# Kernel optimization log

Measured on AMD Instinct MI355X. Metric: run time of the kernel, lower is better.

Reference implementation:

```python
import jax, jax.numpy as jnp
import numpy as np

N_ENTS = 100000
N_EDGES = 200000
H = 256
NUM_RELS = 200  # embedding table has 2*NUM_RELS rows
TYPE_DIM = H // 4


def layer_norm(x, g, b, eps=1e-5):
    m = jnp.mean(x, axis=-1, keepdims=True)
    v = jnp.var(x, axis=-1, keepdims=True)
    return (x - m) * jax.lax.rsqrt(v + eps) * g + b


def setup_inputs() -> dict:
    key = jax.random.key(0)
    ks = jax.random.split(key, 20)
    s = 0.02  # xavier-ish scale for weights
    return {
        "node_emb": jax.random.normal(ks[0], (N_ENTS, H), jnp.float32),
        "h_prev": jax.random.normal(ks[1], (N_ENTS, H), jnp.float32),
        "type_emb": jax.random.normal(ks[2], (2 * NUM_RELS, TYPE_DIM), jnp.float32) * s,
        "W_edge": jax.random.normal(ks[3], (2 * H + TYPE_DIM, H), jnp.float32) * s,
        "b_edge": jnp.zeros((H,), jnp.float32),
        "ln_edge_g": jnp.ones((H,), jnp.float32),
        "ln_edge_b": jnp.zeros((H,), jnp.float32),
        "W_gate": jax.random.normal(ks[4], (2 * H, H), jnp.float32) * s,
        "b_gate": jnp.zeros((H,), jnp.float32),
        "ln_gate_g": jnp.ones((H,), jnp.float32),
        "ln_gate_b": jnp.zeros((H,), jnp.float32),
        "W_ih": jax.random.normal(ks[5], (3 * H, H), jnp.float32) * s,
        "W_hh": jax.random.normal(ks[6], (3 * H, H), jnp.float32) * s,
        "b_ih": jnp.zeros((3 * H,), jnp.float32),
        "b_hh": jnp.zeros((3 * H,), jnp.float32),
        "ln_gru_g": jnp.ones((H,), jnp.float32),
        "ln_gru_b": jnp.zeros((H,), jnp.float32),
        "src": jax.random.randint(ks[7], (N_EDGES,), 0, N_ENTS, jnp.int32),
        "dst": jax.random.randint(ks[8], (N_EDGES,), 0, N_ENTS, jnp.int32),
        "edge_types": jax.random.randint(ks[9], (N_EDGES,), 0, 2 * NUM_RELS, jnp.int32),
    }


def reference(node_emb, h_prev, type_emb, W_edge, b_edge, ln_edge_g, ln_edge_b,
              W_gate, b_gate, ln_gate_g, ln_gate_b,
              W_ih, W_hh, b_ih, b_hh, ln_gru_g, ln_gru_b,
              src, dst, edge_types):
    # --- EdgeFeatureExtractor: gather + edge MLP (dropout=eval identity) ---
    edge_in = jnp.concatenate(
        [node_emb[src], node_emb[dst], type_emb[edge_types]], axis=1)  # [E, 2H+H/4]
    edge_feat = jax.nn.relu(
        layer_norm(edge_in @ W_edge + b_edge, ln_edge_g, ln_edge_b))  # [E, H]

    # --- create_edge_enhanced_nodes: scatter-mean over dst ---
    agg = jax.ops.segment_sum(edge_feat, dst, num_segments=N_ENTS)  # [N, H]
    cnt = jax.ops.segment_sum(jnp.ones((edge_feat.shape[0],), edge_feat.dtype),
                              dst, num_segments=N_ENTS)
    edge_enh = agg / jnp.clip(cnt, 1.0)[:, None]

    # --- DualStreamProcessor fusion ---
    gate = jax.nn.sigmoid(layer_norm(
        jnp.concatenate([node_emb, edge_enh], axis=1) @ W_gate + b_gate,
        ln_gate_g, ln_gate_b))
    fused = gate * node_emb + (1.0 - gate) * edge_enh
    x = 0.2 * node_emb + 0.8 * fused

    # --- EnhancedGRUCell: torch GRUCell + LayerNorm + 0.3*h residual ---
    gi = x @ W_ih.T + b_ih      # [N, 3H]
    gh = h_prev @ W_hh.T + b_hh  # [N, 3H]
    gi_r, gi_z, gi_n = jnp.split(gi, 3, axis=1)
    gh_r, gh_z, gh_n = jnp.split(gh, 3, axis=1)
    r = jax.nn.sigmoid(gi_r + gh_r)
    z = jax.nn.sigmoid(gi_z + gh_z)
    n = jnp.tanh(gi_n + r * gh_n)
    h = (1.0 - z) * n + z * h_prev
    h = layer_norm(h, ln_gru_g, ln_gru_b) + 0.3 * h_prev
    return h
```

## Files before the change

### kernel.cpp

```cpp
#include <hip/hip_runtime.h>
#include <hip/hip_bf16.h>
#include <hip/hip_fp16.h>

#define H 256
#define TYPE_DIM 64
#define EIN (2*H + TYPE_DIM)
#define N_ENTS 100000
#define N_EDGES 200000
#define EPB 32
#define NPB 64
#define KE 576
#define LDE 584
#define LDF 260
#define LDA 520
#define LDH 264
#define LDF2 260

typedef __hip_bfloat16 bf16;
typedef short bf16x8 __attribute__((ext_vector_type(8)));
typedef float f32x4 __attribute__((ext_vector_type(4)));

__device__ __forceinline__ unsigned short f2b(float f) {
    union { float f; unsigned int u; } v; v.f = f;
    unsigned int u = v.u;
    return (unsigned short)((u + 0x7FFFu + ((u >> 16) & 1u)) >> 16);
}
__device__ __forceinline__ unsigned int pack2(float a, float b) {
    return (unsigned int)f2b(a) | ((unsigned int)f2b(b) << 16);
}
__device__ __forceinline__ float u2f(unsigned short u) {
    union { unsigned int i; float f; } t; t.i = ((unsigned int)u) << 16; return t.f;
}
__device__ __forceinline__ float sigm(float x) { return 1.0f / (1.0f + __expf(-x)); }

__device__ __forceinline__ void atomic_pk_f16(void* p, unsigned int v) {
    asm volatile("global_atomic_pk_add_f16 %0, %1, off" :: "v"(p), "v"(v) : "memory");
}

__device__ __forceinline__ bf16x8 cvt8(const float* p) {
    f32x4 a = *(const f32x4*)p;
    f32x4 b = *(const f32x4*)(p + 4);
    union { bf16 h[8]; bf16x8 v; } u;
    u.h[0] = __float2bfloat16(a[0]); u.h[1] = __float2bfloat16(a[1]);
    u.h[2] = __float2bfloat16(a[2]); u.h[3] = __float2bfloat16(a[3]);
    u.h[4] = __float2bfloat16(b[0]); u.h[5] = __float2bfloat16(b[1]);
    u.h[6] = __float2bfloat16(b[2]); u.h[7] = __float2bfloat16(b[3]);
    return u.v;
}

__global__ void transpose_we(const float* __restrict__ W,
                             unsigned short* __restrict__ WE) {
    int c = blockIdx.x;
    for (int j = threadIdx.x; j < KE; j += 256)
        WE[(size_t)c * KE + j] = f2b(W[(size_t)j * H + c]);
}

__global__ void transpose_wg(const float* __restrict__ W,
                             unsigned short* __restrict__ WG) {
    int c = blockIdx.x;
    for (int k = threadIdx.x; k < 2 * H; k += 256)
        WG[(size_t)c * (2 * H) + k] = f2b(W[(size_t)k * H + c]);
}

__global__ void cast_gru(const float* __restrict__ Wih, const float* __restrict__ Whh,
                         unsigned short* __restrict__ WTih,
                         unsigned short* __restrict__ WThh, int do_hh) {
    int j = blockIdx.x;
    int k = threadIdx.x;
    WTih[(size_t)j * H + k] = f2b(Wih[(size_t)j * H + k]);
    if (do_hh) WThh[(size_t)j * H + k] = f2b(Whh[(size_t)j * H + k]);
}

__global__ __launch_bounds__(256) void edge_mfma(
    const float* __restrict__ node_emb, const float* __restrict__ type_emb,
    const unsigned short* __restrict__ WE,
    const float* __restrict__ b_edge,
    const float* __restrict__ ln_g, const float* __restrict__ ln_b,
    const int* __restrict__ src, const int* __restrict__ dst,
    const int* __restrict__ et,
    unsigned char* __restrict__ aggb,
    unsigned int* __restrict__ cntw) {
    __shared__ __align__(16) unsigned short ein[EPB * LDE];
    __shared__ int sidx[EPB], didx[EPB], tidx[EPB];

    const int tid = threadIdx.x;
    const int e0 = blockIdx.x * EPB;
    const int lane = tid & 63;
    const int w = tid >> 6;
    const int l15 = lane & 15;
    const int l4 = lane >> 4;

    if (tid < EPB) {
        sidx[tid] = src[e0 + tid];
        didx[tid] = dst[e0 + tid];
        tidx[tid] = et[e0 + tid];
    }
    __syncthreads();

    {
        const int half = tid >> 7;
        const int tt = tid & 127;
        #pragma unroll 4
        for (int e = 0; e < EPB; e++) {
            const int n = half ? didx[e] : sidx[e];
            const float2 v = *(const float2*)(node_emb + (size_t)n * H + 2 * tt);
            *(unsigned int*)&ein[e * LDE + half * 256 + 2 * tt] = pack2(v.x, v.y);
        }
        #pragma unroll
        for (int i = tid; i < EPB * 32; i += 256) {
            const int e = i >> 5, j = i & 31;
            const float2 v = *(const float2*)(type_emb + (size_t)tidx[e] * TYPE_DIM + 2 * j);
            *(unsigned int*)&ein[e * LDE + 512 + 2 * j] = pack2(v.x, v.y);
        }
    }
    __syncthreads();

    f32x4 acc[2][4];
    #pragma unroll
    for (int mt = 0; mt < 2; mt++)
        #pragma unroll
        for (int nt = 0; nt < 4; nt++)
            acc[mt][nt] = (f32x4){0.f, 0.f, 0.f, 0.f};

    const int colbase = w * 64;
    const unsigned short* A0 = &ein[l15 * LDE + l4 * 8];
    const unsigned short* A1 = &ein[(16 + l15) * LDE + l4 * 8];
    const unsigned short* B0 = WE + (size_t)(colbase + l15) * KE + l4 * 8;
    const unsigned short* B1 = B0 + 16 * KE;
    const unsigned short* B2 = B0 + 32 * KE;
    const unsigned short* B3 = B0 + 48 * KE;

    for (int ks = 0; ks < KE / 32; ks++) {
        const int o = ks * 32;
        bf16x8 a0 = __builtin_bit_cast(bf16x8, *(const uint4*)(A0 + o));
        bf16x8 a1 = __builtin_bit_cast(bf16x8, *(const uint4*)(A1 + o));
        bf16x8 b0 = __builtin_bit_cast(bf16x8, *(const uint4*)(B0 + o));
        bf16x8 b1 = __builtin_bit_cast(bf16x8, *(const uint4*)(B1 + o));
        bf16x8 b2 = __builtin_bit_cast(bf16x8, *(const uint4*)(B2 + o));
        bf16x8 b3 = __builtin_bit_cast(bf16x8, *(const uint4*)(B3 + o));
        acc[0][0] = __builtin_amdgcn_mfma_f32_16x16x32_bf16(a0, b0, acc[0][0], 0, 0, 0);
        acc[0][1] = __builtin_amdgcn_mfma_f32_16x16x32_bf16(a0, b1, acc[0][1], 0, 0, 0);
        acc[0][2] = __builtin_amdgcn_mfma_f32_16x16x32_bf16(a0, b2, acc[0][2], 0, 0, 0);
        acc[0][3] = __builtin_amdgcn_mfma_f32_16x16x32_bf16(a0, b3, acc[0][3], 0, 0, 0);
        acc[1][0] = __builtin_amdgcn_mfma_f32_16x16x32_bf16(a1, b0, acc[1][0], 0, 0, 0);
        acc[1][1] = __builtin_amdgcn_mfma_f32_16x16x32_bf16(a1, b1, acc[1][1], 0, 0, 0);
        acc[1][2] = __builtin_amdgcn_mfma_f32_16x16x32_bf16(a1, b2, acc[1][2], 0, 0, 0);
        acc[1][3] = __builtin_amdgcn_mfma_f32_16x16x32_bf16(a1, b3, acc[1][3], 0, 0, 0);
    }

    __syncthreads();
    float* fout = (float*)&ein[0];

    float bias[4];
    #pragma unroll
    for (int nt = 0; nt < 4; nt++) bias[nt] = b_edge[colbase + nt * 16 + l15];
    #pragma unroll
    for (int mt = 0; mt < 2; mt++)
        #pragma unroll
        for (int nt = 0; nt < 4; nt++)
            #pragma unroll
            for (int r = 0; r < 4; r++) {
                int row = mt * 16 + l4 * 4 + r;
                fout[row * LDF + colbase + nt * 16 + l15] = acc[mt][nt][r] + bias[nt];
            }
    __syncthreads();

    const float4 gv = *(const float4*)(ln_g + 4 * lane);
    const float4 bv = *(const float4*)(ln_b + 4 * lane);
    for (int rr = 0; rr < 8; rr++) {
        const int row = w * 8 + rr;
        f32x4 v = *(const f32x4*)&fout[row * LDF + 4 * lane];
        float s1 = v[0] + v[1] + v[2] + v[3];
        float s2 = v[0] * v[0] + v[1] * v[1] + v[2] * v[2] + v[3] * v[3];
        #pragma unroll
        for (int o = 32; o > 0; o >>= 1) {
            s1 += __shfl_down(s1, o, 64);
            s2 += __shfl_down(s2, o, 64);
        }
        const float m = __shfl(s1, 0, 64) * (1.0f / (float)H);
        const float q = __shfl(s2, 0, 64) * (1.0f / (float)H);
        const float is = rsqrtf(fmaxf(q - m * m, 0.0f) + 1e-5f);
        float y0 = fmaxf((v[0] - m) * is * gv.x + bv.x, 0.0f);
        float y1 = fmaxf((v[1] - m) * is * gv.y + bv.y, 0.0f);
        float y2 = fmaxf((v[2] - m) * is * gv.z + bv.z, 0.0f);
        float y3 = fmaxf((v[3] - m) * is * gv.w + bv.w, 0.0f);
        __half2 h01 = __floats2half2_rn(y0, y1);
        __half2 h23 = __floats2half2_rn(y2, y3);
        unsigned char* dp = aggb + (size_t)didx[row] * 1024 + lane * 8;
        atomic_pk_f16(dp,     __builtin_bit_cast(unsigned int, h01));
        atomic_pk_f16(dp + 4, __builtin_bit_cast(unsigned int, h23));
    }
    if (tid < EPB) {
        int d = didx[tid];
        atomicAdd(&cntw[d >> 2], 1u << ((d & 3) * 8));
    }
}

template<bool SHH>
__global__ __launch_bounds__(512, 2) void node_mfma(
    const float* __restrict__ node_emb, const float* __restrict__ h_prev,
    const unsigned short* __restrict__ WG, const float* __restrict__ b_gate,
    const float* __restrict__ lng_g, const float* __restrict__ lng_b,
    const unsigned short* __restrict__ WTih, const unsigned short* __restrict__ WThh,
    const float* __restrict__ Whh_f32,
    const float* __restrict__ b_ih, const float* __restrict__ b_hh,
    const float* __restrict__ lnr_g, const float* __restrict__ lnr_b,
    const unsigned int* __restrict__ cntw,
    float* __restrict__ out) {
    __shared__ __align__(16) unsigned short Aga[NPB * LDA];
    __shared__ __align__(16) unsigned short shr[NPB * LDH];
    __shared__ float rc[NPB];

    const int tid = threadIdx.x;
    const int n0 = blockIdx.x * NPB;
    const int lane = tid & 63;
    const int w = tid >> 6;
    const int l15 = lane & 15, l4 = lane >> 4;

    if (tid < NPB) {
        int n = n0 + tid;
        float c = 1.0f;
        if (n < N_ENTS) {
            unsigned int cw = cntw[n >> 2];
            c = (float)((cw >> ((n & 3) * 8)) & 0xFFu);
        }
        rc[tid] = 1.0f / fmaxf(c, 1.0f);
    }
    __syncthreads();

    const unsigned char* aggb = (const unsigned char*)out;

    for (int i = tid; i < NPB * 128; i += 512) {
        int row = i >> 7, c2 = (i & 127) * 2;
        int nr = n0 + row;
        size_t gn = (size_t)(nr < N_ENTS ? nr : 0);
        float2 xv = *(const float2*)(node_emb + gn * H + c2);
        unsigned int eu = *(const unsigned int*)(aggb + gn * 1024 + c2 * 2);
        float2 ev = __half22float2(__builtin_bit_cast(__half2, eu));
        float r = rc[row];
        *(unsigned int*)&Aga[row * LDA + c2]       = pack2(xv.x, xv.y);
        *(unsigned int*)&Aga[row * LDA + 256 + c2] = pack2(ev.x * r, ev.y * r);
    }
    __syncthreads();

    {
        f32x4 acc[4][2];
        #pragma unroll
        for (int m = 0; m < 4; m++)
            #pragma unroll
            for (int nt = 0; nt < 2; nt++) acc[m][nt] = (f32x4){0.f, 0.f, 0.f, 0.f};
        const unsigned short* Ab = &Aga[l15 * LDA + l4 * 8];
        const unsigned short* B0 = WG + (size_t)(w * 32 + l15) * (2 * H) + l4 * 8;
        const unsigned short* B1 = B0 + 16 * (2 * H);
        #pragma unroll 4
        for (int ks = 0; ks < 16; ks++) {
            const int o = ks * 32;
            bf16x8 b0 = __builtin_bit_cast(bf16x8, *(const uint4*)(B0 + o));
            bf16x8 b1 = __builtin_bit_cast(bf16x8, *(const uint4*)(B1 + o));
            #pragma unroll
            for (int m = 0; m < 4; m++) {
                bf16x8 a = __builtin_bit_cast(bf16x8, *(const uint4*)(Ab + m * 16 * LDA + o));
                acc[m][0] = __builtin_amdgcn_mfma_f32_16x16x32_bf16(a, b0, acc[m][0], 0, 0, 0);
                acc[m][1] = __builtin_amdgcn_mfma_f32_16x16x32_bf16(a, b1, acc[m][1], 0, 0, 0);
            }
        }
        const float bg0 = b_gate[w * 32 + l15];
        const float bg1 = b_gate[w * 32 + 16 + l15];
        #pragma unroll
        for (int m = 0; m < 4; m++)
            #pragma unroll
            for (int r = 0; r < 4; r++) {
                int row = m * 16 + l4 * 4 + r;
                shr[row * LDH + w * 32 + l15]      = f2b(acc[m][0][r] + bg0);
                shr[row * LDH + w * 32 + 16 + l15] = f2b(acc[m][1][r] + bg1);
            }
    }
    __syncthreads();

    {
        const float4 g4 = *(const float4*)(lng_g + 4 * lane);
        const float4 b4 = *(const float4*)(lng_b + 4 * lane);
        for (int rr = 0; rr < 8; rr++) {
            const int row = w * 8 + rr;
            short4 us = *(const short4*)&shr[row * LDH + 4 * lane];
            float u0 = u2f((unsigned short)us.x), u1 = u2f((unsigned short)us.y);
            float u2 = u2f((unsigned short)us.z), u3 = u2f((unsigned short)us.w);
            float s1 = u0 + u1 + u2 + u3;
            float s2 = u0 * u0 + u1 * u1 + u2 * u2 + u3 * u3;
            #pragma unroll
            for (int o = 32; o > 0; o >>= 1) {
                s1 += __shfl_down(s1, o, 64);
                s2 += __shfl_down(s2, o, 64);
            }
            const float m = __shfl(s1, 0, 64) * (1.0f / (float)H);
            const float q = __shfl(s2, 0, 64) * (1.0f / (float)H);
            const float is = rsqrtf(fmaxf(q - m * m, 0.0f) + 1e-5f);
            short4 xr = *(const short4*)&Aga[row * LDA + 4 * lane];
            short4 er = *(const short4*)&Aga[row * LDA + 256 + 4 * lane];
            float xv[4] = {u2f((unsigned short)xr.x), u2f((unsigned short)xr.y),
                           u2f((unsigned short)xr.z), u2f((unsigned short)xr.w)};
            float ev[4] = {u2f((unsigned short)er.x), u2f((unsigned short)er.y),
                           u2f((unsigned short)er.z), u2f((unsigned short)er.w)};
            float uu[4] = {u0, u1, u2, u3};
            float gl[4] = {g4.x, g4.y, g4.z, g4.w};
            float bl[4] = {b4.x, b4.y, b4.z, b4.w};
            unsigned short xs[4];
            #pragma unroll
            for (int j = 0; j < 4; j++) {
                float gate = sigm((uu[j] - m) * is * gl[j] + bl[j]);
                float fused = gate * xv[j] + (1.0f - gate) * ev[j];
                xs[j] = f2b(0.2f * xv[j] + 0.8f * fused);
            }
            *(unsigned int*)&Aga[row * LDA + 4 * lane]     = (unsigned int)xs[0] | ((unsigned int)xs[1] << 16);
            *(unsigned int*)&Aga[row * LDA + 4 * lane + 2] = (unsigned int)xs[2] | ((unsigned int)xs[3] << 16);
        }
    }
    __syncthreads();

    for (int i = tid; i < NPB * 128; i += 512) {
        int row = i >> 7, c2 = (i & 127) * 2;
        int nr = n0 + row;
        size_t g = (size_t)(nr < N_ENTS ? nr : 0) * H + c2;
        float2 hv = *(const float2*)(h_prev + g);
        *(unsigned int*)&shr[row * LDH + c2] = pack2(hv.x, hv.y);
    }
    __syncthreads();

    float hreg[2][4][4];
    #pragma unroll
    for (int p = 0; p < 2; p++) {
        f32x4 aI[3][4], aH[3][4];
        #pragma unroll
        for (int s = 0; s < 3; s++)
            #pragma unroll
            for (int m = 0; m < 4; m++) {
                aI[s][m] = (f32x4){0.f, 0.f, 0.f, 0.f};
                aH[s][m] = (f32x4){0.f, 0.f, 0.f, 0.f};
            }
        const int cl = w * 32 + p * 16 + l15;
        const unsigned short* Xb = &Aga[l15 * LDA + l4 * 8];
        const unsigned short* Pb = &shr[l15 * LDH + l4 * 8];
        const unsigned short* bi0 = WTih + (size_t)(cl) * H + l4 * 8;
        const unsigned short* bi1 = WTih + (size_t)(H + cl) * H + l4 * 8;
        const unsigned short* bi2 = WTih + (size_t)(2 * H + cl) * H + l4 * 8;
        const unsigned short* bh0s = WThh + (size_t)(cl) * H + l4 * 8;
        const unsigned short* bh1s = WThh + (size_t)(H + cl) * H + l4 * 8;
        const unsigned short* bh2s = WThh + (size_t)(2 * H + cl) * H + l4 * 8;
        const float* fh0 = Whh_f32 + (size_t)(cl) * H + l4 * 8;
        const float* fh1 = Whh_f32 + (size_t)(H + cl) * H + l4 * 8;
        const float* fh2 = Whh_f32 + (size_t)(2 * H + cl) * H + l4 * 8;
        #pragma unroll 4
        for (int ks = 0; ks < 8; ks++) {
            const int o = ks * 32;
            bf16x8 bI[3], bH[3];
            bI[0] = __builtin_bit_cast(bf16x8, *(const uint4*)(bi0 + o));
            bI[1] = __builtin_bit_cast(bf16x8, *(const uint4*)(bi1 + o));
            bI[2] = __builtin_bit_cast(bf16x8, *(const uint4*)(bi2 + o));
            if (SHH) {
                bH[0] = __builtin_bit_cast(bf16x8, *(const uint4*)(bh0s + o));
                bH[1] = __builtin_bit_cast(bf16x8, *(const uint4*)(bh1s + o));
                bH[2] = __builtin_bit_cast(bf16x8, *(const uint4*)(bh2s + o));
            } else {
                bH[0] = cvt8(fh0 + o);
                bH[1] = cvt8(fh1 + o);
                bH[2] = cvt8(fh2 + o);
            }
            #pragma unroll
            for (int m = 0; m < 4; m++) {
                bf16x8 ax = __builtin_bit_cast(bf16x8, *(const uint4*)(Xb + m * 16 * LDA + o));
                bf16x8 ah = __builtin_bit_cast(bf16x8, *(const uint4*)(Pb + m * 16 * LDH + o));
                #pragma unroll
                for (int s = 0; s < 3; s++) {
                    aI[s][m] = __builtin_amdgcn_mfma_f32_16x16x32_bf16(ax, bI[s], aI[s][m], 0, 0, 0);
                    aH[s][m] = __builtin_amdgcn_mfma_f32_16x16x32_bf16(ah, bH[s], aH[s][m], 0, 0, 0);
                }
            }
        }
        const float bi_0 = b_ih[cl], bi_1 = b_ih[H + cl], bi_2 = b_ih[2 * H + cl];
        const float bh_0 = b_hh[cl], bh_1 = b_hh[H + cl], bh_2 = b_hh[2 * H + cl];
        #pragma unroll
        for (int m = 0; m < 4; m++)
            #pragma unroll
            for (int r = 0; r < 4; r++) {
                const int row = m * 16 + l4 * 4 + r;
                int nr = n0 + row; if (nr >= N_ENTS) nr = N_ENTS - 1;
                float rg = sigm(aI[0][m][r] + bi_0 + aH[0][m][r] + bh_0);
                float zg = sigm(aI[1][m][r] + bi_1 + aH[1][m][r] + bh_1);
                float nn = tanhf(aI[2][m][r] + bi_2 + rg * (aH[2][m][r] + bh_2));
                float hpv = h_prev[(size_t)nr * H + cl];
                hreg[p][m][r] = (1.0f - zg) * nn + zg * hpv;
            }
    }
    __syncthreads();

    float* hb = (float*)&Aga[0];
    #pragma unroll
    for (int p = 0; p < 2; p++) {
        const int cl = w * 32 + p * 16 + l15;
        #pragma unroll
        for (int m = 0; m < 4; m++)
            #pragma unroll
            for (int r = 0; r < 4; r++)
                hb[(m * 16 + l4 * 4 + r) * LDF2 + cl] = hreg[p][m][r];
    }
    __syncthreads();

    {
        const float4 g4 = *(const float4*)(lnr_g + 4 * lane);
        const float4 b4 = *(const float4*)(lnr_b + 4 * lane);
        for (int rr = 0; rr < 8; rr++) {
            const int row = w * 8 + rr;
            const int nr = n0 + row;
            f32x4 hv = *(const f32x4*)&hb[row * LDF2 + 4 * lane];
            float s1 = hv[0] + hv[1] + hv[2] + hv[3];
            float s2 = hv[0] * hv[0] + hv[1] * hv[1] + hv[2] * hv[2] + hv[3] * hv[3];
            #pragma unroll
            for (int o = 32; o > 0; o >>= 1) {
                s1 += __shfl_down(s1, o, 64);
                s2 += __shfl_down(s2, o, 64);
            }
            const float m = __shfl(s1, 0, 64) * (1.0f / (float)H);
            const float q = __shfl(s2, 0, 64) * (1.0f / (float)H);
            const float is = rsqrtf(fmaxf(q - m * m, 0.0f) + 1e-5f);
            if (nr < N_ENTS) {
                const float4 hp4 = *(const float4*)(h_prev + (size_t)nr * H + 4 * lane);
                float4 o4;
                o4.x = (hv[0] - m) * is * g4.x + b4.x + 0.3f * hp4.x;
                o4.y = (hv[1] - m) * is * g4.y + b4.y + 0.3f * hp4.y;
                o4.z = (hv[2] - m) * is * g4.z + b4.z + 0.3f * hp4.z;
                o4.w = (hv[3] - m) * is * g4.w + b4.w + 0.3f * hp4.w;
                *(float4*)(out + (size_t)nr * H + 4 * lane) = o4;
            }
        }
    }
}

extern "C" void kernel_launch(void* const* d_in, const int* in_sizes, int n_in,
                              void* d_out, int out_size, void* d_ws, size_t ws_size,
                              hipStream_t stream) {
    (void)in_sizes; (void)n_in; (void)out_size;
    const float* node_emb  = (const float*)d_in[0];
    const float* h_prev    = (const float*)d_in[1];
    const float* type_emb  = (const float*)d_in[2];
    const float* W_edge    = (const float*)d_in[3];
    const float* b_edge    = (const float*)d_in[4];
    const float* ln_edge_g = (const float*)d_in[5];
    const float* ln_edge_b = (const float*)d_in[6];
    const float* W_gate    = (const float*)d_in[7];
    const float* b_gate    = (const float*)d_in[8];
    const float* ln_gate_g = (const float*)d_in[9];
    const float* ln_gate_b = (const float*)d_in[10];
    const float* W_ih      = (const float*)d_in[11];
    const float* W_hh      = (const float*)d_in[12];
    const float* b_ih      = (const float*)d_in[13];
    const float* b_hh      = (const float*)d_in[14];
    const float* ln_gru_g  = (const float*)d_in[15];
    const float* ln_gru_b  = (const float*)d_in[16];
    const int*   src       = (const int*)d_in[17];
    const int*   dst       = (const int*)d_in[18];
    const int*   et        = (const int*)d_in[19];
    float* out = (float*)d_out;

    char* ws = (char*)d_ws;
    unsigned int* cntw  = (unsigned int*)ws;
    unsigned short* WE   = (unsigned short*)(ws + 100000);
    unsigned short* WG   = (unsigned short*)(ws + 100000);
    unsigned short* WTih = (unsigned short*)(ws + 362144);
    unsigned short* WThh = (unsigned short*)(ws + 755360);
    const bool big = ws_size >= (size_t)1148576;

    hipMemsetAsync(cntw, 0, 100000, stream);
    hipMemsetAsync(out, 0, (size_t)N_ENTS * H * sizeof(float), stream);

    hipLaunchKernelGGL(transpose_we, dim3(256), dim3(256), 0, stream, W_edge, WE);

    hipLaunchKernelGGL(edge_mfma, dim3(N_EDGES / EPB), dim3(256), 0, stream,
                       node_emb, type_emb, WE, b_edge, ln_edge_g, ln_edge_b,
                       src, dst, et, (unsigned char*)out, cntw);

    hipLaunchKernelGGL(transpose_wg, dim3(256), dim3(256), 0, stream, W_gate, WG);
    hipLaunchKernelGGL(cast_gru, dim3(768), dim3(256), 0, stream,
                       W_ih, W_hh, WTih, WThh, big ? 1 : 0);

    const int nblocks = (N_ENTS + NPB - 1) / NPB;
    if (big) {
        hipLaunchKernelGGL((node_mfma<true>), dim3(nblocks), dim3(512), 0, stream,
                           node_emb, h_prev, WG, b_gate, ln_gate_g, ln_gate_b,
                           WTih, WThh, W_hh, b_ih, b_hh, ln_gru_g, ln_gru_b,
                           cntw, out);
    } else {
        hipLaunchKernelGGL((node_mfma<false>), dim3(nblocks), dim3(512), 0, stream,
                           node_emb, h_prev, WG, b_gate, ln_gate_g, ln_gate_b,
                           WTih, WTih , W_hh, b_ih, b_hh, ln_gru_g, ln_gru_b,
                           cntw, out);
    }
}
```

Before: 1.027 ms.

## Use 1024-thread node blocks with 16 columns per wave and staged GRU gates

The node kernel now runs with 1024 threads (16 waves) per 64-node block. Each wave owns 16 output columns instead of 32, which halves the per-wave accumulators. The GRU matmul is split into two phases: r/z gates first, then the n gate, so fewer accumulator arrays are live at once. The goal is lower register pressure and more waves in flight to hide memory latency. In exchange, each wave issues fewer MFMAs per A-tile LDS read, and launch_bounds(1024,4) may force register spills.

```diff
diff --git a/kernel.cpp b/kernel.cpp
--- a/kernel.cpp
+++ b/kernel.cpp
@@ -197,7 +197,7 @@
 }
 
 template<bool SHH>
-__global__ __launch_bounds__(512, 2) void node_mfma(
+__global__ __launch_bounds__(1024, 4) void node_mfma(
     const float* __restrict__ node_emb, const float* __restrict__ h_prev,
     const unsigned short* __restrict__ WG, const float* __restrict__ b_gate,
     const float* __restrict__ lng_g, const float* __restrict__ lng_b,
@@ -230,7 +230,7 @@
 
     const unsigned char* aggb = (const unsigned char*)out;
 
-    for (int i = tid; i < NPB * 128; i += 512) {
+    for (int i = tid; i < NPB * 128; i += 1024) {
         int row = i >> 7, c2 = (i & 127) * 2;
         int nr = n0 + row;
         size_t gn = (size_t)(nr < N_ENTS ? nr : 0);
@@ -244,35 +244,28 @@
     __syncthreads();
 
     {
-        f32x4 acc[4][2];
-        #pragma unroll
-        for (int m = 0; m < 4; m++)
-            #pragma unroll
-            for (int nt = 0; nt < 2; nt++) acc[m][nt] = (f32x4){0.f, 0.f, 0.f, 0.f};
+        f32x4 acc[4];
+        #pragma unroll
+        for (int m = 0; m < 4; m++) acc[m] = (f32x4){0.f, 0.f, 0.f, 0.f};
         const unsigned short* Ab = &Aga[l15 * LDA + l4 * 8];
-        const unsigned short* B0 = WG + (size_t)(w * 32 + l15) * (2 * H) + l4 * 8;
-        const unsigned short* B1 = B0 + 16 * (2 * H);
+        const unsigned short* B0 = WG + (size_t)(w * 16 + l15) * (2 * H) + l4 * 8;
         #pragma unroll 4
         for (int ks = 0; ks < 16; ks++) {
             const int o = ks * 32;
             bf16x8 b0 = __builtin_bit_cast(bf16x8, *(const uint4*)(B0 + o));
-            bf16x8 b1 = __builtin_bit_cast(bf16x8, *(const uint4*)(B1 + o));
             #pragma unroll
             for (int m = 0; m < 4; m++) {
                 bf16x8 a = __builtin_bit_cast(bf16x8, *(const uint4*)(Ab + m * 16 * LDA + o));
-                acc[m][0] = __builtin_amdgcn_mfma_f32_16x16x32_bf16(a, b0, acc[m][0], 0, 0, 0);
-                acc[m][1] = __builtin_amdgcn_mfma_f32_16x16x32_bf16(a, b1, acc[m][1], 0, 0, 0);
-            }
-        }
-        const float bg0 = b_gate[w * 32 + l15];
-        const float bg1 = b_gate[w * 32 + 16 + l15];
+                acc[m] = __builtin_amdgcn_mfma_f32_16x16x32_bf16(a, b0, acc[m], 0, 0, 0);
+            }
+        }
+        const float bg0 = b_gate[w * 16 + l15];
         #pragma unroll
         for (int m = 0; m < 4; m++)
             #pragma unroll
             for (int r = 0; r < 4; r++) {
                 int row = m * 16 + l4 * 4 + r;
-                shr[row * LDH + w * 32 + l15]      = f2b(acc[m][0][r] + bg0);
-                shr[row * LDH + w * 32 + 16 + l15] = f2b(acc[m][1][r] + bg1);
+                shr[row * LDH + w * 16 + l15] = f2b(acc[m][r] + bg0);
             }
     }
     __syncthreads();
@@ -280,8 +273,8 @@
     {
         const float4 g4 = *(const float4*)(lng_g + 4 * lane);
         const float4 b4 = *(const float4*)(lng_b + 4 * lane);
-        for (int rr = 0; rr < 8; rr++) {
-            const int row = w * 8 + rr;
+        for (int rr = 0; rr < 4; rr++) {
+            const int row = w * 4 + rr;
             short4 us = *(const short4*)&shr[row * LDH + 4 * lane];
             float u0 = u2f((unsigned short)us.x), u1 = u2f((unsigned short)us.y);
             float u2 = u2f((unsigned short)us.z), u3 = u2f((unsigned short)us.w);
@@ -317,7 +310,7 @@
     }
     __syncthreads();
 
-    for (int i = tid; i < NPB * 128; i += 512) {
+    for (int i = tid; i < NPB * 128; i += 1024) {
         int row = i >> 7, c2 = (i & 127) * 2;
         int nr = n0 + row;
         size_t g = (size_t)(nr < N_ENTS ? nr : 0) * H + c2;
@@ -326,90 +319,112 @@
     }
     __syncthreads();
 
-    float hreg[2][4][4];
-    #pragma unroll
-    for (int p = 0; p < 2; p++) {
-        f32x4 aI[3][4], aH[3][4];
-        #pragma unroll
-        for (int s = 0; s < 3; s++)
-            #pragma unroll
-            for (int m = 0; m < 4; m++) {
-                aI[s][m] = (f32x4){0.f, 0.f, 0.f, 0.f};
-                aH[s][m] = (f32x4){0.f, 0.f, 0.f, 0.f};
-            }
-        const int cl = w * 32 + p * 16 + l15;
-        const unsigned short* Xb = &Aga[l15 * LDA + l4 * 8];
-        const unsigned short* Pb = &shr[l15 * LDH + l4 * 8];
+    const int cl = w * 16 + l15;
+    const unsigned short* Xb = &Aga[l15 * LDA + l4 * 8];
+    const unsigned short* Pb = &shr[l15 * LDH + l4 * 8];
+
+    float rg[4][4], zg[4][4];
+    {
+        f32x4 aIr[4], aIz[4], aHr[4], aHz[4];
+        #pragma unroll
+        for (int m = 0; m < 4; m++) {
+            aIr[m] = (f32x4){0.f, 0.f, 0.f, 0.f}; aIz[m] = (f32x4){0.f, 0.f, 0.f, 0.f};
+            aHr[m] = (f32x4){0.f, 0.f, 0.f, 0.f}; aHz[m] = (f32x4){0.f, 0.f, 0.f, 0.f};
+        }
         const unsigned short* bi0 = WTih + (size_t)(cl) * H + l4 * 8;
         const unsigned short* bi1 = WTih + (size_t)(H + cl) * H + l4 * 8;
-        const unsigned short* bi2 = WTih + (size_t)(2 * H + cl) * H + l4 * 8;
         const unsigned short* bh0s = WThh + (size_t)(cl) * H + l4 * 8;
         const unsigned short* bh1s = WThh + (size_t)(H + cl) * H + l4 * 8;
-        const unsigned short* bh2s = WThh + (size_t)(2 * H + cl) * H + l4 * 8;
         const float* fh0 = Whh_f32 + (size_t)(cl) * H + l4 * 8;
         const float* fh1 = Whh_f32 + (size_t)(H + cl) * H + l4 * 8;
+        #pragma unroll 4
+        for (int ks = 0; ks < 8; ks++) {
+            const int o = ks * 32;
+            bf16x8 vI0 = __builtin_bit_cast(bf16x8, *(const uint4*)(bi0 + o));
+            bf16x8 vI1 = __builtin_bit_cast(bf16x8, *(const uint4*)(bi1 + o));
+            bf16x8 vH0, vH1;
+            if (SHH) {
+                vH0 = __builtin_bit_cast(bf16x8, *(const uint4*)(bh0s + o));
+                vH1 = __builtin_bit_cast(bf16x8, *(const uint4*)(bh1s + o));
+            } else {
+                vH0 = cvt8(fh0 + o);
+                vH1 = cvt8(fh1 + o);
+            }
+            #pragma unroll
+            for (int m = 0; m < 4; m++) {
+                bf16x8 ax = __builtin_bit_cast(bf16x8, *(const uint4*)(Xb + m * 16 * LDA + o));
+                bf16x8 ah = __builtin_bit_cast(bf16x8, *(const uint4*)(Pb + m * 16 * LDH + o));
+                aIr[m] = __builtin_amdgcn_mfma_f32_16x16x32_bf16(ax, vI0, aIr[m], 0, 0, 0);
+                aIz[m] = __builtin_amdgcn_mfma_f32_16x16x32_bf16(ax, vI1, aIz[m], 0, 0, 0);
+                aHr[m] = __builtin_amdgcn_mfma_f32_16x16x32_bf16(ah, vH0, aHr[m], 0, 0, 0);
+                aHz[m] = __builtin_amdgcn_mfma_f32_16x16x32_bf16(ah, vH1, aHz[m], 0, 0, 0);
+            }
+        }
+        const float bi_0 = b_ih[cl], bi_1 = b_ih[H + cl];
+        const float bh_0 = b_hh[cl], bh_1 = b_hh[H + cl];
+        #pragma unroll
+        for (int m = 0; m < 4; m++)
+            #pragma unroll
+            for (int r = 0; r < 4; r++) {
+                rg[m][r] = sigm(aIr[m][r] + bi_0 + aHr[m][r] + bh_0);
+                zg[m][r] = sigm(aIz[m][r] + bi_1 + aHz[m][r] + bh_1);
+            }
+    }
+
+    float hreg[4][4];
+    {
+        f32x4 aIn[4], aHn[4];
+        #pragma unroll
+        for (int m = 0; m < 4; m++) {
+            aIn[m] = (f32x4){0.f, 0.f, 0.f, 0.f};
+            aHn[m] = (f32x4){0.f, 0.f, 0.f, 0.f};
+        }
+        const unsigned short* bi2 = WTih + (size_t)(2 * H + cl) * H + l4 * 8;
+        const unsigned short* bh2s = WThh + (size_t)(2 * H + cl) * H + l4 * 8;
         const float* fh2 = Whh_f32 + (size_t)(2 * H + cl) * H + l4 * 8;
         #pragma unroll 4
         for (int ks = 0; ks < 8; ks++) {
             const int o = ks * 32;
-            bf16x8 bI[3], bH[3];
-            bI[0] = __builtin_bit_cast(bf16x8, *(const uint4*)(bi0 + o));
-            bI[1] = __builtin_bit_cast(bf16x8, *(const uint4*)(bi1 + o));
-            bI[2] = __builtin_bit_cast(bf16x8, *(const uint4*)(bi2 + o));
-            if (SHH) {
-                bH[0] = __builtin_bit_cast(bf16x8, *(const uint4*)(bh0s + o));
-                bH[1] = __builtin_bit_cast(bf16x8, *(const uint4*)(bh1s + o));
-                bH[2] = __builtin_bit_cast(bf16x8, *(const uint4*)(bh2s + o));
-            } else {
-                bH[0] = cvt8(fh0 + o);
-                bH[1] = cvt8(fh1 + o);
-                bH[2] = cvt8(fh2 + o);
-            }
+            bf16x8 vI2 = __builtin_bit_cast(bf16x8, *(const uint4*)(bi2 + o));
+            bf16x8 vH2;
+            if (SHH) vH2 = __builtin_bit_cast(bf16x8, *(const uint4*)(bh2s + o));
+            else     vH2 = cvt8(fh2 + o);
             #pragma unroll
             for (int m = 0; m < 4; m++) {
                 bf16x8 ax = __builtin_bit_cast(bf16x8, *(const uint4*)(Xb + m * 16 * LDA + o));
                 bf16x8 ah = __builtin_bit_cast(bf16x8, *(const uint4*)(Pb + m * 16 * LDH + o));
-                #pragma unroll
-                for (int s = 0; s < 3; s++) {
-                    aI[s][m] = __builtin_amdgcn_mfma_f32_16x16x32_bf16(ax, bI[s], aI[s][m], 0, 0, 0);
-                    aH[s][m] = __builtin_amdgcn_mfma_f32_16x16x32_bf16(ah, bH[s], aH[s][m], 0, 0, 0);
-                }
-            }
-        }
-        const float bi_0 = b_ih[cl], bi_1 = b_ih[H + cl], bi_2 = b_ih[2 * H + cl];
-        const float bh_0 = b_hh[cl], bh_1 = b_hh[H + cl], bh_2 = b_hh[2 * H + cl];
+                aIn[m] = __builtin_amdgcn_mfma_f32_16x16x32_bf16(ax, vI2, aIn[m], 0, 0, 0);
+                aHn[m] = __builtin_amdgcn_mfma_f32_16x16x32_bf16(ah, vH2, aHn[m], 0, 0, 0);
+            }
+        }
+        const float bi_2 = b_ih[2 * H + cl];
+        const float bh_2 = b_hh[2 * H + cl];
         #pragma unroll
         for (int m = 0; m < 4; m++)
             #pragma unroll
             for (int r = 0; r < 4; r++) {
                 const int row = m * 16 + l4 * 4 + r;
                 int nr = n0 + row; if (nr >= N_ENTS) nr = N_ENTS - 1;
-                float rg = sigm(aI[0][m][r] + bi_0 + aH[0][m][r] + bh_0);
-                float zg = sigm(aI[1][m][r] + bi_1 + aH[1][m][r] + bh_1);
-                float nn = tanhf(aI[2][m][r] + bi_2 + rg * (aH[2][m][r] + bh_2));
+                float nn = tanhf(aIn[m][r] + bi_2 + rg[m][r] * (aHn[m][r] + bh_2));
                 float hpv = h_prev[(size_t)nr * H + cl];
-                hreg[p][m][r] = (1.0f - zg) * nn + zg * hpv;
+                hreg[m][r] = (1.0f - zg[m][r]) * nn + zg[m][r] * hpv;
             }
     }
     __syncthreads();
 
     float* hb = (float*)&Aga[0];
     #pragma unroll
-    for (int p = 0; p < 2; p++) {
-        const int cl = w * 32 + p * 16 + l15;
-        #pragma unroll
-        for (int m = 0; m < 4; m++)
-            #pragma unroll
-            for (int r = 0; r < 4; r++)
-                hb[(m * 16 + l4 * 4 + r) * LDF2 + cl] = hreg[p][m][r];
-    }
+    for (int m = 0; m < 4; m++)
+        #pragma unroll
+        for (int r = 0; r < 4; r++)
+            hb[(m * 16 + l4 * 4 + r) * LDF2 + cl] = hreg[m][r];
     __syncthreads();
 
     {
         const float4 g4 = *(const float4*)(lnr_g + 4 * lane);
         const float4 b4 = *(const float4*)(lnr_b + 4 * lane);
-        for (int rr = 0; rr < 8; rr++) {
-            const int row = w * 8 + rr;
+        for (int rr = 0; rr < 4; rr++) {
+            const int row = w * 4 + rr;
             const int nr = n0 + row;
             f32x4 hv = *(const f32x4*)&hb[row * LDF2 + 4 * lane];
             float s1 = hv[0] + hv[1] + hv[2] + hv[3];
@@ -484,12 +499,12 @@
 
     const int nblocks = (N_ENTS + NPB - 1) / NPB;
     if (big) {
-        hipLaunchKernelGGL((node_mfma<true>), dim3(nblocks), dim3(512), 0, stream,
+        hipLaunchKernelGGL((node_mfma<true>), dim3(nblocks), dim3(1024), 0, stream,
                            node_emb, h_prev, WG, b_gate, ln_gate_g, ln_gate_b,
                            WTih, WThh, W_hh, b_ih, b_hh, ln_gru_g, ln_gru_b,
                            cntw, out);
     } else {
-        hipLaunchKernelGGL((node_mfma<false>), dim3(nblocks), dim3(512), 0, stream,
+        hipLaunchKernelGGL((node_mfma<false>), dim3(nblocks), dim3(1024), 0, stream,
                            node_emb, h_prev, WG, b_gate, ln_gate_g, ln_gate_b,
                            WTih, WTih , W_hh, b_ih, b_hh, ln_gru_g, ln_gru_b,
                            cntw, out);
```

Result: faster. 990.3 us (-3.6%).
